# Kernel optimization log

Measured on AMD Instinct MI355X. Metric: run time of the kernel, lower is better.

Reference implementation:

```python
import jax, jax.numpy as jnp
import numpy as np

NUM_UNFOLDS = 6
TAU = 1.0
ELAPSED = 1.0

def setup_inputs() -> dict:
    key = jax.random.key(0)
    k1, k2, k3, k4 = jax.random.split(key, 4)
    B, D_IN, UNITS = 32768, 256, 512
    inputs = jax.random.normal(k1, (B, D_IN), dtype=jnp.float32)
    hidden_state = jax.random.normal(k2, (B, UNITS), dtype=jnp.float32)
    # glorot-ish scaling for kernel, orthogonal-ish (scaled normal) for recurrent
    kernel = jax.random.normal(k3, (D_IN, UNITS), dtype=jnp.float32) * (1.0 / np.sqrt(D_IN))
    recurrent_kernel = jax.random.normal(k4, (UNITS, UNITS), dtype=jnp.float32) * (1.0 / np.sqrt(UNITS))
    bias = jnp.zeros((UNITS,), dtype=jnp.float32)
    scale = jnp.ones((UNITS,), dtype=jnp.float32)
    return {"inputs": inputs, "hidden_state": hidden_state, "kernel": kernel,
            "recurrent_kernel": recurrent_kernel, "bias": bias, "scale": scale}

def _dfdt(x, h, kernel, recurrent_kernel, bias, scale):
    # dh = scale * tanh(x@K + h@R + b) - tau*h
    pre = x @ kernel + h @ recurrent_kernel + bias
    dh_in = scale * jnp.tanh(pre)
    return dh_in - h * TAU

def _rk4_step(x, h, dt, kernel, recurrent_kernel, bias, scale):
    k1 = _dfdt(x, h, kernel, recurrent_kernel, bias, scale)
    k2 = _dfdt(x, h + k1 * (dt * 0.5), kernel, recurrent_kernel, bias, scale)
    k3 = _dfdt(x, h + k2 * (dt * 0.5), kernel, recurrent_kernel, bias, scale)
    k4 = _dfdt(x, h + k3 * dt, kernel, recurrent_kernel, bias, scale)
    return h + dt * (k1 + 2.0 * k2 + 2.0 * k3 + k4) / 6.0

def reference(inputs, hidden_state, kernel, recurrent_kernel, bias, scale):
    dt = ELAPSED / NUM_UNFOLDS
    def body(h, _):
        return _rk4_step(inputs, h, dt, kernel, recurrent_kernel, bias, scale), None
    h, _ = jax.lax.scan(body, hidden_state, None, length=NUM_UNFOLDS)
    return h
```

## Files before the change

kernel.cpp:

```cpp
#include <hip/hip_runtime.h>

typedef unsigned int u32;
typedef unsigned short u16;
typedef __bf16 bf16x8 __attribute__((ext_vector_type(8)));
typedef float f32x16 __attribute__((ext_vector_type(16)));
typedef float f32x4v __attribute__((ext_vector_type(4)));
typedef u32 u32x4 __attribute__((ext_vector_type(4)));
typedef u32 u32x2 __attribute__((ext_vector_type(2)));

#define BATCH    32768
#define DIN      256
#define UNITS    512
#define BM       64
#define NTHREADS 1024
#define NSTEP    6
#define DT       (1.0f/6.0f)
#define TANH_C   2.885390082f
#define SMEM_BYTES (65536 + 65536 + 32768)

__device__ __forceinline__ u16 f2bf(float f) {
  return __builtin_bit_cast(u16, (__bf16)f);
}
__device__ __forceinline__ float bf2f(u16 b) {
  return __builtin_bit_cast(float, (u32)b << 16);
}
__device__ __forceinline__ u32 pk2(float a, float b) {
  return (u32)f2bf(a) | ((u32)f2bf(b) << 16);
}
__device__ __forceinline__ float tanh_pre(float t) {
  float a = __builtin_amdgcn_exp2f(fminf(t, 60.f));
  float r = __builtin_amdgcn_rcpf(a + 1.f);
  return __builtin_fmaf(-2.f, r, 1.f);
}

__global__ void pack_weights(const float* __restrict__ Km, const float* __restrict__ Rm,
                             u16* __restrict__ Kp, u16* __restrict__ Rp) {
  int c = blockIdx.x * 256 + threadIdx.x;
  if (c < 32768) {
    int n = c & 511, g = c >> 9;
    u32x4 p;
#pragma unroll
    for (int i = 0; i < 4; ++i) {
      u16 lo = f2bf(Rm[(g * 8 + 2 * i) * 512 + n] * TANH_C);
      u16 hh = f2bf(Rm[(g * 8 + 2 * i + 1) * 512 + n] * TANH_C);
      p[i] = (u32)lo | ((u32)hh << 16);
    }
    ((u32x4*)Rp)[c] = p;
  } else {
    int c2 = c - 32768;
    int n = c2 & 511, g = c2 >> 9;
    u32x4 p;
#pragma unroll
    for (int i = 0; i < 4; ++i) {
      u16 lo = f2bf(Km[(g * 8 + 2 * i) * 512 + n] * TANH_C);
      u16 hh = f2bf(Km[(g * 8 + 2 * i + 1) * 512 + n] * TANH_C);
      p[i] = (u32)lo | ((u32)hh << 16);
    }
    ((u32x4*)Kp)[c2] = p;
  }
}

__global__ __launch_bounds__(NTHREADS, 4)
void ctrnn_fused(const float* __restrict__ X, const float* __restrict__ H0,
                 const u16* __restrict__ Kp, const u16* __restrict__ Rp,
                 const float* __restrict__ bias, const float* __restrict__ scale,
                 float* __restrict__ out) {
  extern __shared__ char smem[];
  char* heA  = smem;
  float* h1L = (float*)(smem + 65536);
  u32* xkbL1 = (u32*)(smem + 131072);

  const int tid  = threadIdx.x;
  const int lane = tid & 63;
  const int wv   = tid >> 6;
  const int ln   = lane & 31, hi = lane >> 5;
  const long r0  = (long)blockIdx.x * BM;

  const int jc   = wv * 32 + ln;
  const int aoff = lane * 16;
  const int hB   = wv * 2048 + ((ln >> 4) << 10) + (((ln >> 3) & 1) << 9)
                 + ((ln & 7) << 1) + hi * 64;

  {
    const f32x4v* X4 = (const f32x4v*)(X + r0 * DIN);
#pragma unroll
    for (int i = 0; i < 4; ++i) {
      int flat = i * NTHREADS + tid;
      int m = flat >> 6, c4 = flat & 63;
      f32x4v v = X4[m * 64 + c4];
      u32x2 p;
      p.x = pk2(v.x, v.y);
      p.y = pk2(v.z, v.w);
      int addr = (m >> 5) * 16384 + (c4 >> 2) * 1024 + ((c4 >> 1) & 1) * 512
               + (m & 31) * 16 + (c4 & 1) * 8;
      *(u32x2*)(heA + addr) = p;
    }
  }

  const float scl = scale[jc];

  float h0[16];
#pragma unroll
  for (int r = 0; r < 16; ++r) {
    int m = (r & 3) + ((r >> 2) << 3) + hi * 4;
    h0[r] = H0[(r0 + m) * UNITS + jc];
    h1L[r * NTHREADS + tid] = H0[(r0 + m + 32) * UNITS + jc];
  }

  __syncthreads();

  {
    f32x16 pre0, pre1;
    {
      float b = bias[jc] * TANH_C;
#pragma unroll
      for (int r = 0; r < 16; ++r) { pre0[r] = b; pre1[r] = b; }
    }
    const u32x4* Kp4 = (const u32x4*)Kp;
#pragma unroll 2
    for (int kb = 0; kb < 16; ++kb) {
      bf16x8 a0 = __builtin_bit_cast(bf16x8, *(const u32x4*)(heA + kb * 1024 + aoff));
      bf16x8 a1 = __builtin_bit_cast(bf16x8, *(const u32x4*)(heA + 16384 + kb * 1024 + aoff));
      bf16x8 bb = __builtin_bit_cast(bf16x8, Kp4[(kb * 2 + hi) * 512 + jc]);
      pre0 = __builtin_amdgcn_mfma_f32_32x32x16_bf16(a0, bb, pre0, 0, 0, 0);
      pre1 = __builtin_amdgcn_mfma_f32_32x32x16_bf16(a1, bb, pre1, 0, 0, 0);
    }
    u32 xkbP0t[8];
#pragma unroll
    for (int i = 0; i < 8; ++i) {
      xkbP0t[i] = pk2(pre0[2 * i], pre0[2 * i + 1]);
      xkbL1[i * NTHREADS + tid] = pk2(pre1[2 * i], pre1[2 * i + 1]);
    }
    __syncthreads();

#pragma unroll
    for (int r = 0; r < 16; ++r) {
      int mm = (r & 3) + ((r >> 2) << 3);
      *(u16*)(heA + hB + mm * 16)         = f2bf(h0[r]);
      *(u16*)(heA + hB + mm * 16 + 32768) = f2bf(h1L[r * NTHREADS + tid]);
    }
    __syncthreads();

    const u32x4* Rp4 = (const u32x4*)Rp;
    u32 accP0[8], accP1[8];
    u32 xkbP0[8];
#pragma unroll
    for (int i = 0; i < 8; ++i) xkbP0[i] = xkbP0t[i];

#pragma unroll 1
    for (int it = 0; it < NSTEP * 4; ++it) {
      const int ev = it & 3;
      const float wk = (ev == 1 || ev == 2) ? 2.f : 1.f;
      const float ce = (ev < 2) ? (DT * 0.5f) : DT;
      const bool ev0 = (ev == 0), ev3 = (ev == 3);
      const bool last = (it == NSTEP * 4 - 1);

      f32x16 p0, p1;
#pragma unroll
      for (int i = 0; i < 8; ++i) {
        u32 q0 = xkbP0[i];
        u32 q1 = xkbL1[i * NTHREADS + tid];
        p0[2 * i]     = bf2f((u16)(q0 & 0xffffu));
        p0[2 * i + 1] = bf2f((u16)(q0 >> 16));
        p1[2 * i]     = bf2f((u16)(q1 & 0xffffu));
        p1[2 * i + 1] = bf2f((u16)(q1 >> 16));
      }
#pragma unroll 2
      for (int kb = 0; kb < 32; ++kb) {
        bf16x8 a0 = __builtin_bit_cast(bf16x8, *(const u32x4*)(heA + kb * 1024 + aoff));
        bf16x8 a1 = __builtin_bit_cast(bf16x8, *(const u32x4*)(heA + 32768 + kb * 1024 + aoff));
        bf16x8 bb = __builtin_bit_cast(bf16x8, Rp4[(kb * 2 + hi) * 512 + jc]);
        p0 = __builtin_amdgcn_mfma_f32_32x32x16_bf16(a0, bb, p0, 0, 0, 0);
        p1 = __builtin_amdgcn_mfma_f32_32x32x16_bf16(a1, bb, p1, 0, 0, 0);
      }

#pragma unroll
      for (int rp = 0; rp < 8; ++rp) {
        int mmA = ((2 * rp) & 3) + (((2 * rp) >> 2) << 3);
        int mmB = ((2 * rp + 1) & 3) + (((2 * rp + 1) >> 2) << 3);
        float he0 = bf2f(*(const u16*)(heA + hB + mmA * 16));
        float he1 = bf2f(*(const u16*)(heA + hB + mmB * 16));
        float k0 = __builtin_fmaf(scl, tanh_pre(p0[2 * rp]),     -he0);
        float k1 = __builtin_fmaf(scl, tanh_pre(p0[2 * rp + 1]), -he1);
        float a0 = (ev0 ? 0.f : bf2f((u16)(accP0[rp] & 0xffffu))) + wk * k0;
        float a1 = (ev0 ? 0.f : bf2f((u16)(accP0[rp] >> 16)))     + wk * k1;
        if (ev3) {
          h0[2 * rp]     += (DT / 6.f) * a0;
          h0[2 * rp + 1] += (DT / 6.f) * a1;
        } else {
          accP0[rp] = pk2(a0, a1);
        }
        p0[2 * rp] = k0; p0[2 * rp + 1] = k1;
      }
#pragma unroll
      for (int rp = 0; rp < 8; ++rp) {
        int mmA = ((2 * rp) & 3) + (((2 * rp) >> 2) << 3);
        int mmB = ((2 * rp + 1) & 3) + (((2 * rp + 1) >> 2) << 3);
        float he0 = bf2f(*(const u16*)(heA + hB + mmA * 16 + 32768));
        float he1 = bf2f(*(const u16*)(heA + hB + mmB * 16 + 32768));
        float k0 = __builtin_fmaf(scl, tanh_pre(p1[2 * rp]),     -he0);
        float k1 = __builtin_fmaf(scl, tanh_pre(p1[2 * rp + 1]), -he1);
        float a0 = (ev0 ? 0.f : bf2f((u16)(accP1[rp] & 0xffffu))) + wk * k0;
        float a1 = (ev0 ? 0.f : bf2f((u16)(accP1[rp] >> 16)))     + wk * k1;
        if (ev3) {
          float hv0 = h1L[(2 * rp) * NTHREADS + tid]     + (DT / 6.f) * a0;
          float hv1 = h1L[(2 * rp + 1) * NTHREADS + tid] + (DT / 6.f) * a1;
          h1L[(2 * rp) * NTHREADS + tid]     = hv0;
          h1L[(2 * rp + 1) * NTHREADS + tid] = hv1;
        } else {
          accP1[rp] = pk2(a0, a1);
        }
        p1[2 * rp] = k0; p1[2 * rp + 1] = k1;
      }
      __syncthreads();

      if (!last) {
#pragma unroll
        for (int r = 0; r < 16; ++r) {
          int mm = (r & 3) + ((r >> 2) << 3);
          float v0 = ev3 ? h0[r] : h0[r] + ce * p0[r];
          *(u16*)(heA + hB + mm * 16) = f2bf(v0);
          float hv = h1L[r * NTHREADS + tid];
          float v1 = ev3 ? hv : hv + ce * p1[r];
          *(u16*)(heA + hB + mm * 16 + 32768) = f2bf(v1);
        }
        __syncthreads();
      }
    }
  }

#pragma unroll
  for (int r = 0; r < 16; ++r) {
    int m = (r & 3) + ((r >> 2) << 3) + hi * 4;
    out[(r0 + m) * UNITS + jc]      = h0[r];
    out[(r0 + m + 32) * UNITS + jc] = h1L[r * NTHREADS + tid];
  }
}

extern "C" void kernel_launch(void* const* d_in, const int* in_sizes, int n_in,
                              void* d_out, int out_size, void* d_ws, size_t ws_size,
                              hipStream_t stream) {
  const float* X     = (const float*)d_in[0];
  const float* H0    = (const float*)d_in[1];
  const float* Km    = (const float*)d_in[2];
  const float* Rm    = (const float*)d_in[3];
  const float* bias  = (const float*)d_in[4];
  const float* scale = (const float*)d_in[5];
  float* out = (float*)d_out;

  u16* Rp = (u16*)d_ws;
  u16* Kp = Rp + UNITS * UNITS;

  (void)hipFuncSetAttribute((const void*)ctrnn_fused,
                            hipFuncAttributeMaxDynamicSharedMemorySize, SMEM_BYTES);

  pack_weights<<<192, 256, 0, stream>>>(Km, Rm, Kp, Rp);
  ctrnn_fused<<<BATCH / BM, NTHREADS, SMEM_BYTES, stream>>>(X, H0, Kp, Rp, bias, scale, out);
}
```

Baseline: 675.6 us.

## Remap waves to 32x64 output tiles and XOR-swizzle shared A operand

After: 710.2 us. 1.05x slower.

```diff
diff --git a/kernel.cpp b/kernel.cpp
--- a/kernel.cpp
+++ b/kernel.cpp
@@ -73,13 +73,19 @@
   const int tid  = threadIdx.x;
   const int lane = tid & 63;
   const int wv   = tid >> 6;
+  const int wm   = wv >> 3, wn = wv & 7;
   const int ln   = lane & 31, hi = lane >> 5;
   const long r0  = (long)blockIdx.x * BM;
 
-  const int jc   = wv * 32 + ln;
-  const int aoff = lane * 16;
-  const int hB   = wv * 2048 + ((ln >> 4) << 10) + (((ln >> 3) & 1) << 9)
-                 + ((ln & 7) << 1) + hi * 64;
+  const int jc0  = wn * 64 + ln;
+  const int jc1  = jc0 + 32;
+  const int aoff = lane << 4;
+  const int Abase = wm * 32768;
+  const int AbaseX = wm * 16384;
+  const int chunk0 = wn * 4 + (ln >> 4);
+  const int cb0 = wm * 32768 + chunk0 * 1024 + (((ln >> 3) & 1) << 9) + ((ln & 7) << 1);
+  const int U0  = ((hi << 2) ^ (chunk0 & 7)) << 4;
+  const int U1  = U0 ^ 32;
 
   {
     const f32x4v* X4 = (const f32x4v*)(X + r0 * DIN);
@@ -91,20 +97,22 @@
       u32x2 p;
       p.x = pk2(v.x, v.y);
       p.y = pk2(v.z, v.w);
-      int addr = (m >> 5) * 16384 + (c4 >> 2) * 1024 + ((c4 >> 1) & 1) * 512
-               + (m & 31) * 16 + (c4 & 1) * 8;
+      int chunk = c4 >> 2;
+      int block = ((c4 >> 1) & 1) * 32 + (m & 31);
+      int addr = (m >> 5) * 16384 + chunk * 1024
+               + ((block ^ (chunk & 7)) << 4) + (c4 & 1) * 8;
       *(u32x2*)(heA + addr) = p;
     }
   }
 
-  const float scl = scale[jc];
+  const float scl0 = scale[jc0], scl1 = scale[jc1];
 
   float h0[16];
 #pragma unroll
   for (int r = 0; r < 16; ++r) {
-    int m = (r & 3) + ((r >> 2) << 3) + hi * 4;
-    h0[r] = H0[(r0 + m) * UNITS + jc];
-    h1L[r * NTHREADS + tid] = H0[(r0 + m + 32) * UNITS + jc];
+    int m = (r & 3) + ((r >> 2) << 3) + hi * 4 + wm * 32;
+    h0[r] = H0[(r0 + m) * UNITS + jc0];
+    h1L[r * NTHREADS + tid] = H0[(r0 + m) * UNITS + jc1];
   }
 
   __syncthreads();
@@ -112,18 +120,19 @@
   {
     f32x16 pre0, pre1;
     {
-      float b = bias[jc] * TANH_C;
-#pragma unroll
-      for (int r = 0; r < 16; ++r) { pre0[r] = b; pre1[r] = b; }
+      float b0 = bias[jc0] * TANH_C, b1 = bias[jc1] * TANH_C;
+#pragma unroll
+      for (int r = 0; r < 16; ++r) { pre0[r] = b0; pre1[r] = b1; }
     }
     const u32x4* Kp4 = (const u32x4*)Kp;
 #pragma unroll 2
     for (int kb = 0; kb < 16; ++kb) {
-      bf16x8 a0 = __builtin_bit_cast(bf16x8, *(const u32x4*)(heA + kb * 1024 + aoff));
-      bf16x8 a1 = __builtin_bit_cast(bf16x8, *(const u32x4*)(heA + 16384 + kb * 1024 + aoff));
-      bf16x8 bb = __builtin_bit_cast(bf16x8, Kp4[(kb * 2 + hi) * 512 + jc]);
-      pre0 = __builtin_amdgcn_mfma_f32_32x32x16_bf16(a0, bb, pre0, 0, 0, 0);
-      pre1 = __builtin_amdgcn_mfma_f32_32x32x16_bf16(a1, bb, pre1, 0, 0, 0);
+      bf16x8 a = __builtin_bit_cast(bf16x8,
+          *(const u32x4*)(heA + AbaseX + kb * 1024 + (aoff ^ ((kb & 7) << 4))));
+      bf16x8 b0 = __builtin_bit_cast(bf16x8, Kp4[(kb * 2 + hi) * 512 + jc0]);
+      bf16x8 b1 = __builtin_bit_cast(bf16x8, Kp4[(kb * 2 + hi) * 512 + jc1]);
+      pre0 = __builtin_amdgcn_mfma_f32_32x32x16_bf16(a, b0, pre0, 0, 0, 0);
+      pre1 = __builtin_amdgcn_mfma_f32_32x32x16_bf16(a, b1, pre1, 0, 0, 0);
     }
     u32 xkbP0t[8];
 #pragma unroll
@@ -136,8 +145,8 @@
 #pragma unroll
     for (int r = 0; r < 16; ++r) {
       int mm = (r & 3) + ((r >> 2) << 3);
-      *(u16*)(heA + hB + mm * 16)         = f2bf(h0[r]);
-      *(u16*)(heA + hB + mm * 16 + 32768) = f2bf(h1L[r * NTHREADS + tid]);
+      *(u16*)(heA + cb0 + ((mm << 4) ^ U0))        = f2bf(h0[r]);
+      *(u16*)(heA + cb0 + 2048 + ((mm << 4) ^ U1)) = f2bf(h1L[r * NTHREADS + tid]);
     }
     __syncthreads();
 
@@ -167,21 +176,22 @@
       }
 #pragma unroll 2
       for (int kb = 0; kb < 32; ++kb) {
-        bf16x8 a0 = __builtin_bit_cast(bf16x8, *(const u32x4*)(heA + kb * 1024 + aoff));
-        bf16x8 a1 = __builtin_bit_cast(bf16x8, *(const u32x4*)(heA + 32768 + kb * 1024 + aoff));
-        bf16x8 bb = __builtin_bit_cast(bf16x8, Rp4[(kb * 2 + hi) * 512 + jc]);
-        p0 = __builtin_amdgcn_mfma_f32_32x32x16_bf16(a0, bb, p0, 0, 0, 0);
-        p1 = __builtin_amdgcn_mfma_f32_32x32x16_bf16(a1, bb, p1, 0, 0, 0);
+        bf16x8 a = __builtin_bit_cast(bf16x8,
+            *(const u32x4*)(heA + Abase + kb * 1024 + (aoff ^ ((kb & 7) << 4))));
+        bf16x8 b0 = __builtin_bit_cast(bf16x8, Rp4[(kb * 2 + hi) * 512 + jc0]);
+        bf16x8 b1 = __builtin_bit_cast(bf16x8, Rp4[(kb * 2 + hi) * 512 + jc1]);
+        p0 = __builtin_amdgcn_mfma_f32_32x32x16_bf16(a, b0, p0, 0, 0, 0);
+        p1 = __builtin_amdgcn_mfma_f32_32x32x16_bf16(a, b1, p1, 0, 0, 0);
       }
 
 #pragma unroll
       for (int rp = 0; rp < 8; ++rp) {
         int mmA = ((2 * rp) & 3) + (((2 * rp) >> 2) << 3);
         int mmB = ((2 * rp + 1) & 3) + (((2 * rp + 1) >> 2) << 3);
-        float he0 = bf2f(*(const u16*)(heA + hB + mmA * 16));
-        float he1 = bf2f(*(const u16*)(heA + hB + mmB * 16));
-        float k0 = __builtin_fmaf(scl, tanh_pre(p0[2 * rp]),     -he0);
-        float k1 = __builtin_fmaf(scl, tanh_pre(p0[2 * rp + 1]), -he1);
+        float he0 = bf2f(*(const u16*)(heA + cb0 + ((mmA << 4) ^ U0)));
+        float he1 = bf2f(*(const u16*)(heA + cb0 + ((mmB << 4) ^ U0)));
+        float k0 = __builtin_fmaf(scl0, tanh_pre(p0[2 * rp]),     -he0);
+        float k1 = __builtin_fmaf(scl0, tanh_pre(p0[2 * rp + 1]), -he1);
         float a0 = (ev0 ? 0.f : bf2f((u16)(accP0[rp] & 0xffffu))) + wk * k0;
         float a1 = (ev0 ? 0.f : bf2f((u16)(accP0[rp] >> 16)))     + wk * k1;
         if (ev3) {
@@ -196,10 +206,10 @@
       for (int rp = 0; rp < 8; ++rp) {
         int mmA = ((2 * rp) & 3) + (((2 * rp) >> 2) << 3);
         int mmB = ((2 * rp + 1) & 3) + (((2 * rp + 1) >> 2) << 3);
-        float he0 = bf2f(*(const u16*)(heA + hB + mmA * 16 + 32768));
-        float he1 = bf2f(*(const u16*)(heA + hB + mmB * 16 + 32768));
-        float k0 = __builtin_fmaf(scl, tanh_pre(p1[2 * rp]),     -he0);
-        float k1 = __builtin_fmaf(scl, tanh_pre(p1[2 * rp + 1]), -he1);
+        float he0 = bf2f(*(const u16*)(heA + cb0 + 2048 + ((mmA << 4) ^ U1)));
+        float he1 = bf2f(*(const u16*)(heA + cb0 + 2048 + ((mmB << 4) ^ U1)));
+        float k0 = __builtin_fmaf(scl1, tanh_pre(p1[2 * rp]),     -he0);
+        float k1 = __builtin_fmaf(scl1, tanh_pre(p1[2 * rp + 1]), -he1);
         float a0 = (ev0 ? 0.f : bf2f((u16)(accP1[rp] & 0xffffu))) + wk * k0;
         float a1 = (ev0 ? 0.f : bf2f((u16)(accP1[rp] >> 16)))     + wk * k1;
         if (ev3) {
@@ -219,10 +229,10 @@
         for (int r = 0; r < 16; ++r) {
           int mm = (r & 3) + ((r >> 2) << 3);
           float v0 = ev3 ? h0[r] : h0[r] + ce * p0[r];
-          *(u16*)(heA + hB + mm * 16) = f2bf(v0);
+          *(u16*)(heA + cb0 + ((mm << 4) ^ U0)) = f2bf(v0);
           float hv = h1L[r * NTHREADS + tid];
           float v1 = ev3 ? hv : hv + ce * p1[r];
-          *(u16*)(heA + hB + mm * 16 + 32768) = f2bf(v1);
+          *(u16*)(heA + cb0 + 2048 + ((mm << 4) ^ U1)) = f2bf(v1);
         }
         __syncthreads();
       }
@@ -231,9 +241,9 @@
 
 #pragma unroll
   for (int r = 0; r < 16; ++r) {
-    int m = (r & 3) + ((r >> 2) << 3) + hi * 4;
-    out[(r0 + m) * UNITS + jc]      = h0[r];
-    out[(r0 + m + 32) * UNITS + jc] = h1L[r * NTHREADS + tid];
+    int m = (r & 3) + ((r >> 2) << 3) + hi * 4 + wm * 32;
+    out[(r0 + m) * UNITS + jc0] = h0[r];
+    out[(r0 + m) * UNITS + jc1] = h1L[r * NTHREADS + tid];
   }
 }
 
```
